# Performance work log

Hardware: AMD Instinct MI355X
Metric: run time of the kernel (lower is better)

## Reference

```python
import jax, jax.numpy as jnp
import numpy as np
from jax import lax

BN_EPS = 1e-5


def ternary_quantize(x):
    # thresholds from global max/min, split range into thirds
    mx, mn = jnp.max(x), jnp.min(x)
    lo = mn + (mx - mn) / 3
    hi = mx - (mx - mn) / 3
    return jnp.where(x < lo, -1.0, jnp.where(x > hi, 1.0, 0.0)).astype(x.dtype)


def noised_tri_conv(x, w):
    # w: [O, I, 3, 3]; bias=False in BasicBlock
    tw = w - jnp.mean(w)
    tq = ternary_quantize(tw)
    out = lax.conv_general_dilated(
        x, tq, window_strides=(1, 1), padding=((1, 1), (1, 1)),
        dimension_numbers=('NCHW', 'OIHW', 'NCHW'))
    # noised_forward: per-pixel conv of a 1x1 patch with padding=1 ->
    # only the center tap of the 3x3 kernel contributes; generated noise
    # weights are unused in the original code (faithful reproduction);
    # result is detached in torch.
    center = tq[:, :, 1, 1]  # [O, I]
    extra = lax.stop_gradient(jnp.einsum('bchw,oc->bohw', x, center))
    return out + extra


def batch_norm_train(x, gamma, beta):
    mean = jnp.mean(x, axis=(0, 2, 3), keepdims=True)
    var = jnp.var(x, axis=(0, 2, 3), keepdims=True)  # biased, as torch BN
    xhat = (x - mean) * lax.rsqrt(var + BN_EPS)
    return xhat * gamma[None, :, None, None] + beta[None, :, None, None]


def setup_inputs() -> dict:
    key = jax.random.key(0)
    k = jax.random.split(key, 7)
    C = 256
    x = jax.random.normal(k[0], (16, C, 56, 56), dtype=jnp.float32)
    w1 = jax.random.normal(k[1], (C, C, 3, 3), dtype=jnp.float32) * 0.05
    w2 = jax.random.normal(k[2], (C, C, 3, 3), dtype=jnp.float32) * 0.05
    g1 = jax.random.uniform(k[3], (C,), dtype=jnp.float32, minval=0.5, maxval=1.5)
    b1 = jax.random.normal(k[4], (C,), dtype=jnp.float32) * 0.1
    g2 = jax.random.uniform(k[5], (C,), dtype=jnp.float32, minval=0.5, maxval=1.5)
    b2 = jax.random.normal(k[6], (C,), dtype=jnp.float32) * 0.1
    return {'x': x, 'w1': w1, 'w2': w2, 'g1': g1, 'b1': b1, 'g2': g2, 'b2': b2}


def reference(x, w1, w2, g1, b1, g2, b2):
    out1 = noised_tri_conv(x, w1)
    out1 = batch_norm_train(out1, g1, b1)
    out1 = jax.nn.relu(out1)
    out2 = noised_tri_conv(out1, w2)
    out2 = batch_norm_train(out2, g2, b2)
    return jax.nn.relu(out1 + out2)
```

## Files before the change

kernel.cpp:

```cpp
#include <hip/hip_runtime.h>

typedef __bf16 bf16;
typedef __bf16 bf16x8 __attribute__((ext_vector_type(8)));
typedef float f32x4 __attribute__((ext_vector_type(4)));

#define NIMG 16
#define CCH 256
#define HH 56
#define HP 58
#define NBLK (NIMG * 14)
#define NPART 896
#define NPOSV (NIMG * HH * HH)
#define WELEMS 589824

typedef const __attribute__((address_space(1))) void* gas1_t;
typedef __attribute__((address_space(3))) void* las3_t;

__device__ __forceinline__ void gload16(const void* g, void* l) {
  __builtin_amdgcn_global_load_lds((gas1_t)g, (las3_t)l, 16, 0, 0);
}


__global__ __launch_bounds__(256) void w_partial(const float* __restrict__ w1,
                                                 const float* __restrict__ w2,
                                                 double* __restrict__ psum,
                                                 float* __restrict__ pmn,
                                                 float* __restrict__ pmx) {
  int b = blockIdx.x;
  int lb = b & 127;
  const float* w = (b >> 7) ? w2 : w1;
  int t = threadIdx.x;
  double s = 0.0;
  float mn = 3.4028235e38f, mx = -3.4028235e38f;
  for (int i = lb * 4608 + t; i < (lb + 1) * 4608; i += 256) {
    float v = w[i];
    s += (double)v;
    mn = fminf(mn, v);
    mx = fmaxf(mx, v);
  }
  __shared__ double sd[256];
  __shared__ float smn[256], smx[256];
  sd[t] = s; smn[t] = mn; smx[t] = mx;
  __syncthreads();
  for (int st = 128; st > 0; st >>= 1) {
    if (t < st) {
      sd[t] += sd[t + st];
      smn[t] = fminf(smn[t], smn[t + st]);
      smx[t] = fmaxf(smx[t], smx[t + st]);
    }
    __syncthreads();
  }
  if (t == 0) { psum[b] = sd[0]; pmn[b] = smn[0]; pmx[b] = smx[0]; }
}

__global__ void w_finalize(const double* __restrict__ psum,
                           const float* __restrict__ pmn,
                           const float* __restrict__ pmx,
                           float* __restrict__ wq) {
  int t = threadIdx.x;
  if (t < 2) {
    double s = 0.0;
    float mn = 3.4028235e38f, mx = -3.4028235e38f;
    for (int b = t * 128; b < (t + 1) * 128; b++) {
      s += psum[b];
      mn = fminf(mn, pmn[b]);
      mx = fmaxf(mx, pmx[b]);
    }
    float mean = (float)(s / (double)WELEMS);
    float tmn = mn - mean, tmx = mx - mean;
    float d = (tmx - tmn) / 3.0f;
    wq[t * 4 + 0] = mean;
    wq[t * 4 + 1] = tmn + d;
    wq[t * 4 + 2] = tmx - d;
  }
}

__global__ __launch_bounds__(256) void w_quant(const float* __restrict__ w1,
                                               const float* __restrict__ w2,
                                               const float* __restrict__ wq,
                                               bf16* __restrict__ btf1,
                                               bf16* __restrict__ btf2) {
  int bid = blockIdx.x;
  int widx = bid / 2304;
  const float* w = widx ? w2 : w1;
  bf16* bt = widx ? btf2 : btf1;
  float mean = wq[widx * 4], lo = wq[widx * 4 + 1], hi = wq[widx * 4 + 2];
  int e = (bid % 2304) * 256 + threadIdx.x;
  int ki = e & 7;
  int l = (e >> 3) & 63;
  int frag = e >> 9;
  int ob = frag & 15;
  int rest = frag >> 4;
  int kk = rest & 1;
  int scc = rest >> 1;
  int cc = scc & 3;
  int s = scc >> 2;
  int o = ob * 16 + (l & 15);
  int c = cc * 64 + kk * 32 + (l >> 4) * 8 + ki;
  float tv = w[(size_t)o * 2304 + c * 9 + s] - mean;
  float q = tv < lo ? -1.f : (tv > hi ? 1.f : 0.f);
  if (s == 4) q *= 2.f;
  bt[e] = (bf16)q;
}

__global__ __launch_bounds__(256) void pad_convert(const float* __restrict__ x,
                                                   bf16* __restrict__ xpad) {
  int bid = blockIdx.x;
  int hp = bid % HP;
  int n = bid / HP;
  int t = threadIdx.x;
  bf16* orow = xpad + (size_t)(n * HP + hp) * HP * CCH;
  bf16x8 z;
#pragma unroll
  for (int q = 0; q < 8; ++q) z[q] = (bf16)0.f;
  if (hp == 0 || hp == HP - 1) {
    for (int j = t; j < HP * 32; j += 256)
      *(bf16x8*)(orow + (size_t)(j >> 5) * CCH + (j & 31) * 8) = z;
    return;
  }
  __shared__ float tile[CCH * 57];
  const float* xb = x + (size_t)n * CCH * (HH * HH) + (size_t)(hp - 1) * HH;
  for (int j = t; j < CCH * 14; j += 256) {
    int c = j / 14, wq = j % 14;
    float4 v = *(const float4*)(xb + (size_t)c * (HH * HH) + wq * 4);
    float* tp = &tile[c * 57 + wq * 4];
    tp[0] = v.x; tp[1] = v.y; tp[2] = v.z; tp[3] = v.w;
  }
  __syncthreads();
  const int cg = t & 31;
  for (int j = t; j < HP * 32; j += 256) {
    int wp = j >> 5;
    bf16x8 ov = z;
    if (wp >= 1 && wp <= HH) {
#pragma unroll
      for (int q = 0; q < 8; ++q) ov[q] = (bf16)tile[(cg * 8 + q) * 57 + (wp - 1)];
    }
    *(bf16x8*)(orow + (size_t)wp * CCH + cg * 8) = ov;
  }
}

template <int MODE>
__global__ __launch_bounds__(512, 2) void conv_gemm(const bf16* __restrict__ xpad,
                                                    const bf16* __restrict__ btf,
                                                    float* __restrict__ part,
                                                    const bf16* __restrict__ v1pad,
                                                    const float* __restrict__ bnp,
                                                    float* __restrict__ outf,
                                                    bf16* __restrict__ outb) {
  __shared__ __align__(16) char smem[116736];
  const int t = threadIdx.x;
  const int lane = t & 63, wv = t >> 6;
  const int wm = wv >> 2, wn = wv & 3;
  const int g = lane >> 4, li = lane & 15;
  const int rawbid = blockIdx.x;
  const int bid = (rawbid & 7) * (NBLK / 8) + (rawbid >> 3);
  const int n = bid / 14, h0 = (bid % 14) * 4;

  f32x4 acc[8][4];
#pragma unroll
  for (int i = 0; i < 8; i++)
#pragma unroll
    for (int j = 0; j < 4; j++) acc[i][j] = f32x4{0.f, 0.f, 0.f, 0.f};

  auto stageA = [&](int cc, int b) {
#pragma unroll
    for (int i = 0; i < 6; ++i) {
      int idx = wv + i * 8;
      int rr = idx >> 3, po = idx & 7;
      int pp = po * 8 + (lane >> 3);
      int gs = (lane & 7) ^ (lane >> 3);
      const bf16* src = xpad + ((size_t)(n * HP + h0 + rr) * HP + pp) * CCH + cc * 64 + gs * 8;
      gload16(src, smem + b * 49152 + rr * 8192 + po * 1024 + lane * 16);
    }
  };

  auto loadB = [&](bf16x8 (&dst)[4], int s, int cc, int kk) {
#pragma unroll
    for (int f = 0; f < 4; ++f) {
      size_t fragidx = (size_t)(((s * 4 + cc) * 2 + kk) * 16 + wn * 4 + f);
      dst[f] = *(const bf16x8*)(btf + fragidx * 512 + lane * 8);
    }
  };

  auto compute_half = [&](const char* Ab, int half, int dh, int dw, int kk,
                          const bf16x8 (&bx)[4]) {
    bf16x8 a[4];
    int rr = 2 * wm + half + dh;
#pragma unroll
    for (int pc = 0; pc < 4; ++pc) {
      int p = pc * 16 + li + dw;
      int sl = (kk * 4 + g) ^ (p & 7);
      a[pc] = *(const bf16x8*)(Ab + rr * 8192 + p * 128 + sl * 16);
    }
#pragma unroll
    for (int pc = 0; pc < 4; ++pc)
#pragma unroll
      for (int fn = 0; fn < 4; ++fn)
        acc[half * 4 + pc][fn] =
          __builtin_amdgcn_mfma_f32_16x16x32_bf16(a[pc], bx[fn], acc[half * 4 + pc][fn], 0, 0, 0);
  };

  stageA(0, 0);
  bf16x8 bS[2][4];
  bf16x8 bB[4];
  loadB(bS[0], 0, 0, 0);
  __syncthreads();

#pragma unroll
  for (int cc = 0; cc < 4; ++cc) {
    const char* Ab = smem + (cc & 1) * 49152;
    if (cc < 3) stageA(cc + 1, (cc + 1) & 1);
#pragma unroll
    for (int s = 0; s < 9; ++s) {
      const int dh = s / 3, dw = s % 3;
      const int cur = (cc * 9 + s) & 1, nxt = cur ^ 1;
      if (s < 8) loadB(bS[nxt], s + 1, cc, 0);
      else if (cc < 3) loadB(bS[nxt], 0, cc + 1, 0);
      loadB(bB, s, cc, 1);
      __builtin_amdgcn_sched_barrier(0);
      __builtin_amdgcn_s_setprio(1);
      compute_half(Ab, 0, dh, dw, 0, bS[cur]);
      compute_half(Ab, 1, dh, dw, 0, bS[cur]);
      compute_half(Ab, 0, dh, dw, 1, bB);
      compute_half(Ab, 1, dh, dw, 1, bB);
      __builtin_amdgcn_s_setprio(0);
    }
    __syncthreads();
  }

  if (MODE == 1 || MODE == 3) {
    float so[2][4] = {{0.f,0.f,0.f,0.f},{0.f,0.f,0.f,0.f}};
    float qo[2][4] = {{0.f,0.f,0.f,0.f},{0.f,0.f,0.f,0.f}};
#pragma unroll
    for (int fm = 0; fm < 8; ++fm) {
      const int rl = fm >> 2, pc = fm & 3;
      const size_t rowoff = (size_t)(n * HH + h0 + 2 * wm + rl) * HH * CCH;
#pragma unroll
      for (int r = 0; r < 4; ++r) {
        int w = pc * 16 + g * 4 + r;
        if (w < HH) {
#pragma unroll
          for (int fn = 0; fn < 4; ++fn) {
            float v = acc[fm][fn][r];
            so[rl][fn] += v;
            qo[rl][fn] += v * v;
            if (MODE == 3) outb[rowoff + (size_t)w * CCH + wn * 64 + fn * 16 + li] = (bf16)v;
          }
        }
      }
    }
#pragma unroll
    for (int rl = 0; rl < 2; ++rl)
#pragma unroll
      for (int fn = 0; fn < 4; ++fn) {
        so[rl][fn] += __shfl_xor(so[rl][fn], 16);
        so[rl][fn] += __shfl_xor(so[rl][fn], 32);
        qo[rl][fn] += __shfl_xor(qo[rl][fn], 16);
        qo[rl][fn] += __shfl_xor(qo[rl][fn], 32);
      }
    if (g == 0) {
#pragma unroll
      for (int rl = 0; rl < 2; ++rl)
#pragma unroll
        for (int fn = 0; fn < 4; ++fn) {
          int o = wn * 64 + fn * 16 + lane;
          size_t prow = (size_t)(bid * 4 + 2 * wm + rl);
          part[(prow * CCH + o) * 2 + 0] = so[rl][fn];
          part[(prow * CCH + o) * 2 + 1] = qo[rl][fn];
        }
    }
  } else {
    float sc[4], bi[4];
#pragma unroll
    for (int fn = 0; fn < 4; ++fn) {
      int o = wn * 64 + fn * 16 + li;
      sc[fn] = bnp[o * 2];
      bi[fn] = bnp[o * 2 + 1];
    }
    float* fsm = (float*)smem;
    const int TS = 3648;
    for (int rl = 0; rl < 2; ++rl) {
      __syncthreads();
      const int row = h0 + 2 * wm + rl;
#pragma unroll
      for (int pc = 0; pc < 4; ++pc) {
        const int fm = rl * 4 + pc;
#pragma unroll
        for (int r = 0; r < 4; ++r) {
          int w = pc * 16 + g * 4 + r;
          if (w < HH) {
#pragma unroll
            for (int fn = 0; fn < 4; ++fn) {
              int o_loc = fn * 16 + li;
              fsm[wv * TS + w * 65 + o_loc] = acc[fm][fn][r] * sc[fn] + bi[fn];
            }
          }
        }
      }
      const bf16* v1row = v1pad + ((size_t)(n * HP + row + 1) * HP + 1) * CCH + wn * 64;
      for (int i = lane; i < HH * 8; i += 64) {
        int w = i >> 3, og = i & 7;
        bf16x8 v1v = *(const bf16x8*)(v1row + (size_t)w * CCH + og * 8);
        float* tp = &fsm[wv * TS + w * 65 + og * 8];
#pragma unroll
        for (int q = 0; q < 8; ++q) {
          float v = tp[q] + (float)v1v[q];
          tp[q] = v > 0.f ? v : 0.f;
        }
      }
      __syncthreads();
#pragma unroll
      for (int tl = 0; tl < 8; ++tl) {
        int wmt = tl >> 2, wnt = tl & 3;
        int orow = h0 + 2 * wmt + rl;
        for (int j = t; j < 4096; j += 512) {
          int oo = j >> 6, w = j & 63;
          if (w < HH)
            outf[(((size_t)n * CCH + wnt * 64 + oo) * HH + orow) * HH + w] = fsm[tl * TS + w * 65 + oo];
        }
      }
    }
  }
}

__global__ __launch_bounds__(256) void fuse2(const bf16* __restrict__ raw,
                                             const bf16* __restrict__ v1pad,
                                             const float* __restrict__ bnp,
                                             float* __restrict__ out) {
  __shared__ float tile[CCH * 57];
  int bid = blockIdx.x;
  int n = bid / HH, h = bid % HH;
  int t = threadIdx.x;
  const bf16* rrow = raw + (size_t)(n * HH + h) * HH * CCH;
  const bf16* vrow = v1pad + ((size_t)(n * HP + h + 1) * HP + 1) * CCH;
  const int cg = t & 31;
  float sc[8], bi[8];
#pragma unroll
  for (int q = 0; q < 8; ++q) {
    sc[q] = bnp[(cg * 8 + q) * 2];
    bi[q] = bnp[(cg * 8 + q) * 2 + 1];
  }
  for (int j = t; j < HH * 32; j += 256) {
    int w = j >> 5;
    bf16x8 r8 = *(const bf16x8*)(rrow + (size_t)w * CCH + cg * 8);
    bf16x8 v8 = *(const bf16x8*)(vrow + (size_t)w * CCH + cg * 8);
#pragma unroll
    for (int q = 0; q < 8; ++q) {
      float v = (float)r8[q] * sc[q] + bi[q] + (float)v8[q];
      tile[(cg * 8 + q) * 57 + w] = v > 0.f ? v : 0.f;
    }
  }
  __syncthreads();
  float* ob = out + (size_t)n * CCH * (HH * HH) + (size_t)h * HH;
  for (int j = t; j < CCH * 14; j += 256) {
    int c = j / 14, wq = j % 14;
    const float* tp = &tile[c * 57 + wq * 4];
    float4 v = {tp[0], tp[1], tp[2], tp[3]};
    *(float4*)(ob + (size_t)c * (HH * HH) + wq * 4) = v;
  }
}

__global__ __launch_bounds__(256) void bn_reduce1(const float* __restrict__ part,
                                                  float* __restrict__ part2) {
  int t = threadIdx.x, b = blockIdx.x;
  float s = 0.f, q = 0.f;
  for (int r = b * 28; r < (b + 1) * 28; r++) {
    s += part[((size_t)r * CCH + t) * 2 + 0];
    q += part[((size_t)r * CCH + t) * 2 + 1];
  }
  part2[((size_t)b * CCH + t) * 2 + 0] = s;
  part2[((size_t)b * CCH + t) * 2 + 1] = q;
}

__global__ __launch_bounds__(256) void bn_reduce2(const float* __restrict__ part2,
                                                  const float* __restrict__ gamma,
                                                  const float* __restrict__ beta,
                                                  float* __restrict__ params) {
  int t = threadIdx.x;
  float s = 0.f, q = 0.f;
  for (int b = 0; b < 32; b++) {
    s += part2[((size_t)b * CCH + t) * 2 + 0];
    q += part2[((size_t)b * CCH + t) * 2 + 1];
  }
  const float inv = 1.f / (float)NPOSV;
  float mean = s * inv;
  float var = q * inv - mean * mean;
  float sc = gamma[t] / sqrtf(var + 1e-5f);
  params[t * 2 + 0] = sc;
  params[t * 2 + 1] = beta[t] - mean * sc;
}

__global__ __launch_bounds__(256) void bn_apply_b(const bf16* __restrict__ rawb,
                                                  const float* __restrict__ params,
                                                  bf16* __restrict__ xpad) {
  int bid = blockIdx.x;
  int hp = bid % HP;
  int n = bid / HP;
  int t = threadIdx.x;
  bf16* orow = xpad + (size_t)(n * HP + hp) * HP * CCH;
  bf16x8 z;
#pragma unroll
  for (int q = 0; q < 8; ++q) z[q] = (bf16)0.f;
  if (hp == 0 || hp == HP - 1) {
    for (int j = t; j < HP * 32; j += 256)
      *(bf16x8*)(orow + (size_t)(j >> 5) * CCH + (j & 31) * 8) = z;
    return;
  }
  const int cg = t & 31, ws8 = t >> 5;
  float sc[8], bi[8];
#pragma unroll
  for (int q = 0; q < 8; ++q) {
    sc[q] = params[(cg * 8 + q) * 2];
    bi[q] = params[(cg * 8 + q) * 2 + 1];
  }
  const bf16* rrow = rawb + (size_t)(n * HH + (hp - 1)) * HH * CCH;
  for (int wp = ws8; wp < HP; wp += 8) {
    bf16x8 ov = z;
    if (wp >= 1 && wp <= HH) {
      bf16x8 r8 = *(const bf16x8*)(rrow + (size_t)(wp - 1) * CCH + cg * 8);
#pragma unroll
      for (int q = 0; q < 8; ++q) {
        float v = (float)r8[q] * sc[q] + bi[q];
        ov[q] = (bf16)(v > 0.f ? v : 0.f);
      }
    }
    *(bf16x8*)(orow + (size_t)wp * CCH + cg * 8) = ov;
  }
}


extern "C" void kernel_launch(void* const* d_in, const int* in_sizes, int n_in,
                              void* d_out, int out_size, void* d_ws, size_t ws_size,
                              hipStream_t stream) {
  const float* x  = (const float*)d_in[0];
  const float* w1 = (const float*)d_in[1];
  const float* w2 = (const float*)d_in[2];
  const float* g1 = (const float*)d_in[3];
  const float* b1 = (const float*)d_in[4];
  const float* g2 = (const float*)d_in[5];
  const float* b2 = (const float*)d_in[6];
  float* out = (float*)d_out;
  char* ws = (char*)d_ws;

  constexpr size_t O_BT1  = 0;
  constexpr size_t O_BT2  = O_BT1 + 1179648;
  constexpr size_t O_XPAD = O_BT2 + 1179648;
  constexpr size_t O_PART = O_XPAD + (size_t)NIMG * HP * HP * CCH * 2 + 65536;
  constexpr size_t O_PSUM = O_PART + (size_t)NPART * CCH * 2 * 4;
  constexpr size_t O_PMN  = O_PSUM + 2048;
  constexpr size_t O_PMX  = O_PMN + 1024;
  constexpr size_t O_WQ   = O_PMX + 1024;
  constexpr size_t O_BNP1 = O_WQ + 256;
  constexpr size_t O_BNP2 = O_BNP1 + 2048;
  constexpr size_t O_PART2 = O_BNP2 + 2048;
  constexpr size_t O_OUT2RAW = O_PART2 + 65536;
  constexpr size_t NEED_BIG = O_OUT2RAW + (size_t)NPOSV * CCH * 2 + 65536;

  bf16* bt1 = (bf16*)(ws + O_BT1);
  bf16* bt2 = (bf16*)(ws + O_BT2);
  bf16* xpad = (bf16*)(ws + O_XPAD);
  bf16* out1pad = (bf16*)(ws + O_XPAD);
  float* part = (float*)(ws + O_PART);
  double* psum = (double*)(ws + O_PSUM);
  float* pmn = (float*)(ws + O_PMN);
  float* pmx = (float*)(ws + O_PMX);
  float* wq = (float*)(ws + O_WQ);
  float* bnp1 = (float*)(ws + O_BNP1);
  float* bnp2 = (float*)(ws + O_BNP2);
  float* part2 = (float*)(ws + O_PART2);
  bf16* out2raw = (bf16*)(ws + O_OUT2RAW);
  bf16* out1rawb = (bf16*)d_out;

  w_partial<<<256, 256, 0, stream>>>(w1, w2, psum, pmn, pmx);
  w_finalize<<<1, 64, 0, stream>>>(psum, pmn, pmx, wq);
  w_quant<<<4608, 256, 0, stream>>>(w1, w2, wq, bt1, bt2);
  pad_convert<<<NIMG * HP, 256, 0, stream>>>(x, xpad);
  conv_gemm<3><<<NBLK, 512, 0, stream>>>(xpad, bt1, part, nullptr, nullptr, nullptr, out1rawb);
  bn_reduce1<<<32, 256, 0, stream>>>(part, part2);
  bn_reduce2<<<1, 256, 0, stream>>>(part2, g1, b1, bnp1);
  bn_apply_b<<<NIMG * HP, 256, 0, stream>>>(out1rawb, bnp1, out1pad);
  if (ws_size >= NEED_BIG) {
    conv_gemm<3><<<NBLK, 512, 0, stream>>>(out1pad, bt2, part, nullptr, nullptr, nullptr, out2raw);
    bn_reduce1<<<32, 256, 0, stream>>>(part, part2);
    bn_reduce2<<<1, 256, 0, stream>>>(part2, g2, b2, bnp2);
    fuse2<<<NIMG * HH, 256, 0, stream>>>(out2raw, out1pad, bnp2, out);
  } else {
    conv_gemm<1><<<NBLK, 512, 0, stream>>>(out1pad, bt2, part, nullptr, nullptr, nullptr, nullptr);
    bn_reduce1<<<32, 256, 0, stream>>>(part, part2);
    bn_reduce2<<<1, 256, 0, stream>>>(part2, g2, b2, bnp2);
    conv_gemm<2><<<NBLK, 512, 0, stream>>>(out1pad, bt2, nullptr, out1pad, bnp2, out, nullptr);
  }
}
```

Measured before the change: 192.0 us.

## Fuse BN statistics and apply into conv kernel via grid-wide spin barrier

Each conv kernel now keeps its accumulators in registers. After computing the tile, all blocks sync on a global atomic counter, the first 32 blocks reduce the partial BN sums, and a second counter barrier follows. Every block then derives the BN scale and bias itself and writes the normalized, ReLU'd result directly: padded bf16 in place for conv1, and the fp32 output with the residual for conv2. This drops the raw bf16 intermediate writes and reads, the separate reduce, apply and fuse kernels, and the conv recompute fallback path. It relies on all 224 blocks being co-resident, otherwise the spin barriers deadlock, and it adds spin-wait latency.

```diff
diff --git a/kernel.cpp b/kernel.cpp
--- a/kernel.cpp
+++ b/kernel.cpp
@@ -12,6 +12,7 @@
 #define NPART 896
 #define NPOSV (NIMG * HH * HH)
 #define WELEMS 589824
+#define NRED 32
 
 typedef const __attribute__((address_space(1))) void* gas1_t;
 typedef __attribute__((address_space(3))) void* las3_t;
@@ -19,6 +20,8 @@
 __device__ __forceinline__ void gload16(const void* g, void* l) {
   __builtin_amdgcn_global_load_lds((gas1_t)g, (las3_t)l, 16, 0, 0);
 }
+
+__global__ void zero_cnt(unsigned* c) { c[threadIdx.x] = 0u; }
 
 
 __global__ __launch_bounds__(256) void w_partial(const float* __restrict__ w1,
@@ -140,13 +143,17 @@
 }
 
 template <int MODE>
-__global__ __launch_bounds__(512, 2) void conv_gemm(const bf16* __restrict__ xpad,
+__global__ __launch_bounds__(512, 2) void conv_coop(const bf16* __restrict__ xpad,
                                                     const bf16* __restrict__ btf,
                                                     float* __restrict__ part,
+                                                    float* __restrict__ part2,
+                                                    const float* __restrict__ gamma,
+                                                    const float* __restrict__ beta,
                                                     const bf16* __restrict__ v1pad,
-                                                    const float* __restrict__ bnp,
+                                                    bf16* __restrict__ outb,
                                                     float* __restrict__ outf,
-                                                    bf16* __restrict__ outb) {
+                                                    unsigned* __restrict__ cnt_a,
+                                                    unsigned* __restrict__ cnt_b) {
   __shared__ __align__(16) char smem[116736];
   const int t = threadIdx.x;
   const int lane = t & 63, wv = t >> 6;
@@ -228,13 +235,12 @@
     __syncthreads();
   }
 
-  if (MODE == 1 || MODE == 3) {
+  {
     float so[2][4] = {{0.f,0.f,0.f,0.f},{0.f,0.f,0.f,0.f}};
     float qo[2][4] = {{0.f,0.f,0.f,0.f},{0.f,0.f,0.f,0.f}};
 #pragma unroll
     for (int fm = 0; fm < 8; ++fm) {
       const int rl = fm >> 2, pc = fm & 3;
-      const size_t rowoff = (size_t)(n * HH + h0 + 2 * wm + rl) * HH * CCH;
 #pragma unroll
       for (int r = 0; r < 4; ++r) {
         int w = pc * 16 + g * 4 + r;
@@ -244,7 +250,6 @@
             float v = acc[fm][fn][r];
             so[rl][fn] += v;
             qo[rl][fn] += v * v;
-            if (MODE == 3) outb[rowoff + (size_t)w * CCH + wn * 64 + fn * 16 + li] = (bf16)v;
           }
         }
       }
@@ -269,14 +274,77 @@
           part[(prow * CCH + o) * 2 + 1] = qo[rl][fn];
         }
     }
+  }
+
+  __syncthreads();
+  if (t == 0) {
+    __threadfence();
+    atomicAdd(cnt_a, 1u);
+  }
+  if (rawbid < NRED) {
+    if (t == 0) {
+      while (atomicAdd(cnt_a, 0u) < (unsigned)NBLK) __builtin_amdgcn_s_sleep(2);
+      __threadfence();
+    }
+    __syncthreads();
+    if (t < 256) {
+      float s = 0.f, q = 0.f;
+      for (int r = rawbid * 28; r < (rawbid + 1) * 28; r++) {
+        s += part[((size_t)r * CCH + t) * 2 + 0];
+        q += part[((size_t)r * CCH + t) * 2 + 1];
+      }
+      part2[((size_t)rawbid * CCH + t) * 2 + 0] = s;
+      part2[((size_t)rawbid * CCH + t) * 2 + 1] = q;
+    }
+    __syncthreads();
+    if (t == 0) {
+      __threadfence();
+      atomicAdd(cnt_b, 1u);
+    }
+  }
+  if (t == 0) {
+    while (atomicAdd(cnt_b, 0u) < (unsigned)NRED) __builtin_amdgcn_s_sleep(2);
+    __threadfence();
+  }
+  __syncthreads();
+
+  float sc[4], bi[4];
+  const float inv = 1.f / (float)NPOSV;
+#pragma unroll
+  for (int fn = 0; fn < 4; ++fn) {
+    int o = wn * 64 + fn * 16 + li;
+    float s = 0.f, q = 0.f;
+    for (int b = 0; b < NRED; ++b) {
+      s += part2[((size_t)b * CCH + o) * 2 + 0];
+      q += part2[((size_t)b * CCH + o) * 2 + 1];
+    }
+    float mean = s * inv;
+    float var = q * inv - mean * mean;
+    float scale = gamma[o] / sqrtf(var + 1e-5f);
+    sc[fn] = scale;
+    bi[fn] = beta[o] - mean * scale;
+  }
+
+  if (MODE == 1) {
+#pragma unroll
+    for (int fm = 0; fm < 8; ++fm) {
+      const int rl = fm >> 2, pc = fm & 3;
+      const int h = h0 + 2 * wm + rl;
+      bf16* obase = outb + ((size_t)(n * HP + h + 1) * HP + 1) * CCH;
+#pragma unroll
+      for (int r = 0; r < 4; ++r) {
+        int w = pc * 16 + g * 4 + r;
+        if (w < HH) {
+#pragma unroll
+          for (int fn = 0; fn < 4; ++fn) {
+            float v = acc[fm][fn][r] * sc[fn] + bi[fn];
+            v = v > 0.f ? v : 0.f;
+            obase[(size_t)w * CCH + wn * 64 + fn * 16 + li] = (bf16)v;
+          }
+        }
+      }
+    }
   } else {
-    float sc[4], bi[4];
-#pragma unroll
-    for (int fn = 0; fn < 4; ++fn) {
-      int o = wn * 64 + fn * 16 + li;
-      sc[fn] = bnp[o * 2];
-      bi[fn] = bnp[o * 2 + 1];
-    }
     float* fsm = (float*)smem;
     const int TS = 3648;
     for (int rl = 0; rl < 2; ++rl) {
@@ -320,111 +388,6 @@
         }
       }
     }
-  }
-}
-
-__global__ __launch_bounds__(256) void fuse2(const bf16* __restrict__ raw,
-                                             const bf16* __restrict__ v1pad,
-                                             const float* __restrict__ bnp,
-                                             float* __restrict__ out) {
-  __shared__ float tile[CCH * 57];
-  int bid = blockIdx.x;
-  int n = bid / HH, h = bid % HH;
-  int t = threadIdx.x;
-  const bf16* rrow = raw + (size_t)(n * HH + h) * HH * CCH;
-  const bf16* vrow = v1pad + ((size_t)(n * HP + h + 1) * HP + 1) * CCH;
-  const int cg = t & 31;
-  float sc[8], bi[8];
-#pragma unroll
-  for (int q = 0; q < 8; ++q) {
-    sc[q] = bnp[(cg * 8 + q) * 2];
-    bi[q] = bnp[(cg * 8 + q) * 2 + 1];
-  }
-  for (int j = t; j < HH * 32; j += 256) {
-    int w = j >> 5;
-    bf16x8 r8 = *(const bf16x8*)(rrow + (size_t)w * CCH + cg * 8);
-    bf16x8 v8 = *(const bf16x8*)(vrow + (size_t)w * CCH + cg * 8);
-#pragma unroll
-    for (int q = 0; q < 8; ++q) {
-      float v = (float)r8[q] * sc[q] + bi[q] + (float)v8[q];
-      tile[(cg * 8 + q) * 57 + w] = v > 0.f ? v : 0.f;
-    }
-  }
-  __syncthreads();
-  float* ob = out + (size_t)n * CCH * (HH * HH) + (size_t)h * HH;
-  for (int j = t; j < CCH * 14; j += 256) {
-    int c = j / 14, wq = j % 14;
-    const float* tp = &tile[c * 57 + wq * 4];
-    float4 v = {tp[0], tp[1], tp[2], tp[3]};
-    *(float4*)(ob + (size_t)c * (HH * HH) + wq * 4) = v;
-  }
-}
-
-__global__ __launch_bounds__(256) void bn_reduce1(const float* __restrict__ part,
-                                                  float* __restrict__ part2) {
-  int t = threadIdx.x, b = blockIdx.x;
-  float s = 0.f, q = 0.f;
-  for (int r = b * 28; r < (b + 1) * 28; r++) {
-    s += part[((size_t)r * CCH + t) * 2 + 0];
-    q += part[((size_t)r * CCH + t) * 2 + 1];
-  }
-  part2[((size_t)b * CCH + t) * 2 + 0] = s;
-  part2[((size_t)b * CCH + t) * 2 + 1] = q;
-}
-
-__global__ __launch_bounds__(256) void bn_reduce2(const float* __restrict__ part2,
-                                                  const float* __restrict__ gamma,
-                                                  const float* __restrict__ beta,
-                                                  float* __restrict__ params) {
-  int t = threadIdx.x;
-  float s = 0.f, q = 0.f;
-  for (int b = 0; b < 32; b++) {
-    s += part2[((size_t)b * CCH + t) * 2 + 0];
-    q += part2[((size_t)b * CCH + t) * 2 + 1];
-  }
-  const float inv = 1.f / (float)NPOSV;
-  float mean = s * inv;
-  float var = q * inv - mean * mean;
-  float sc = gamma[t] / sqrtf(var + 1e-5f);
-  params[t * 2 + 0] = sc;
-  params[t * 2 + 1] = beta[t] - mean * sc;
-}
-
-__global__ __launch_bounds__(256) void bn_apply_b(const bf16* __restrict__ rawb,
-                                                  const float* __restrict__ params,
-                                                  bf16* __restrict__ xpad) {
-  int bid = blockIdx.x;
-  int hp = bid % HP;
-  int n = bid / HP;
-  int t = threadIdx.x;
-  bf16* orow = xpad + (size_t)(n * HP + hp) * HP * CCH;
-  bf16x8 z;
-#pragma unroll
-  for (int q = 0; q < 8; ++q) z[q] = (bf16)0.f;
-  if (hp == 0 || hp == HP - 1) {
-    for (int j = t; j < HP * 32; j += 256)
-      *(bf16x8*)(orow + (size_t)(j >> 5) * CCH + (j & 31) * 8) = z;
-    return;
-  }
-  const int cg = t & 31, ws8 = t >> 5;
-  float sc[8], bi[8];
-#pragma unroll
-  for (int q = 0; q < 8; ++q) {
-    sc[q] = params[(cg * 8 + q) * 2];
-    bi[q] = params[(cg * 8 + q) * 2 + 1];
-  }
-  const bf16* rrow = rawb + (size_t)(n * HH + (hp - 1)) * HH * CCH;
-  for (int wp = ws8; wp < HP; wp += 8) {
-    bf16x8 ov = z;
-    if (wp >= 1 && wp <= HH) {
-      bf16x8 r8 = *(const bf16x8*)(rrow + (size_t)(wp - 1) * CCH + cg * 8);
-#pragma unroll
-      for (int q = 0; q < 8; ++q) {
-        float v = (float)r8[q] * sc[q] + bi[q];
-        ov[q] = (bf16)(v > 0.f ? v : 0.f);
-      }
-    }
-    *(bf16x8*)(orow + (size_t)wp * CCH + cg * 8) = ov;
   }
 }
 
@@ -450,44 +413,27 @@
   constexpr size_t O_PMN  = O_PSUM + 2048;
   constexpr size_t O_PMX  = O_PMN + 1024;
   constexpr size_t O_WQ   = O_PMX + 1024;
-  constexpr size_t O_BNP1 = O_WQ + 256;
-  constexpr size_t O_BNP2 = O_BNP1 + 2048;
-  constexpr size_t O_PART2 = O_BNP2 + 2048;
-  constexpr size_t O_OUT2RAW = O_PART2 + 65536;
-  constexpr size_t NEED_BIG = O_OUT2RAW + (size_t)NPOSV * CCH * 2 + 65536;
+  constexpr size_t O_PART2 = O_WQ + 256;
+  constexpr size_t O_CNT  = O_PART2 + 65536;
 
   bf16* bt1 = (bf16*)(ws + O_BT1);
   bf16* bt2 = (bf16*)(ws + O_BT2);
   bf16* xpad = (bf16*)(ws + O_XPAD);
-  bf16* out1pad = (bf16*)(ws + O_XPAD);
   float* part = (float*)(ws + O_PART);
   double* psum = (double*)(ws + O_PSUM);
   float* pmn = (float*)(ws + O_PMN);
   float* pmx = (float*)(ws + O_PMX);
   float* wq = (float*)(ws + O_WQ);
-  float* bnp1 = (float*)(ws + O_BNP1);
-  float* bnp2 = (float*)(ws + O_BNP2);
   float* part2 = (float*)(ws + O_PART2);
-  bf16* out2raw = (bf16*)(ws + O_OUT2RAW);
-  bf16* out1rawb = (bf16*)d_out;
-
+  unsigned* cnt = (unsigned*)(ws + O_CNT);
+
+  zero_cnt<<<1, 4, 0, stream>>>(cnt);
   w_partial<<<256, 256, 0, stream>>>(w1, w2, psum, pmn, pmx);
   w_finalize<<<1, 64, 0, stream>>>(psum, pmn, pmx, wq);
   w_quant<<<4608, 256, 0, stream>>>(w1, w2, wq, bt1, bt2);
   pad_convert<<<NIMG * HP, 256, 0, stream>>>(x, xpad);
-  conv_gemm<3><<<NBLK, 512, 0, stream>>>(xpad, bt1, part, nullptr, nullptr, nullptr, out1rawb);
-  bn_reduce1<<<32, 256, 0, stream>>>(part, part2);
-  bn_reduce2<<<1, 256, 0, stream>>>(part2, g1, b1, bnp1);
-  bn_apply_b<<<NIMG * HP, 256, 0, stream>>>(out1rawb, bnp1, out1pad);
-  if (ws_size >= NEED_BIG) {
-    conv_gemm<3><<<NBLK, 512, 0, stream>>>(out1pad, bt2, part, nullptr, nullptr, nullptr, out2raw);
-    bn_reduce1<<<32, 256, 0, stream>>>(part, part2);
-    bn_reduce2<<<1, 256, 0, stream>>>(part2, g2, b2, bnp2);
-    fuse2<<<NIMG * HH, 256, 0, stream>>>(out2raw, out1pad, bnp2, out);
-  } else {
-    conv_gemm<1><<<NBLK, 512, 0, stream>>>(out1pad, bt2, part, nullptr, nullptr, nullptr, nullptr);
-    bn_reduce1<<<32, 256, 0, stream>>>(part, part2);
-    bn_reduce2<<<1, 256, 0, stream>>>(part2, g2, b2, bnp2);
-    conv_gemm<2><<<NBLK, 512, 0, stream>>>(out1pad, bt2, nullptr, out1pad, bnp2, out, nullptr);
-  }
-}
+  conv_coop<1><<<NBLK, 512, 0, stream>>>(xpad, bt1, part, part2, g1, b1,
+                                         nullptr, xpad, nullptr, cnt + 0, cnt + 1);
+  conv_coop<2><<<NBLK, 512, 0, stream>>>(xpad, bt2, part, part2, g2, b2,
+                                         xpad, nullptr, out, cnt + 2, cnt + 3);
+}
```

Result: slower. 241.0 us (+25.5%).

## Use 4-wave conv blocks with 128-wide per-wave output tiles, drop fallback path

Applied to the files above, without the earlier changes.

Changes the conv GEMM from 8 waves of 512 threads to 4 waves of 256 threads. Each wave now computes a 128-row by 128-column tile (8x8 MFMA fragments) instead of 128x64, so A fragments from LDS and B fragments are reused across twice as many MFMAs. The cost is 256 accumulator floats per lane plus larger B register buffers, with one block per CU and fewer waves to hide latency. The workspace-size fallback path and the MODE template are removed, so the large-workspace path always runs.

```diff
diff --git a/kernel.cpp b/kernel.cpp
--- a/kernel.cpp
+++ b/kernel.cpp
@@ -139,33 +139,29 @@
   }
 }
 
-template <int MODE>
-__global__ __launch_bounds__(512, 2) void conv_gemm(const bf16* __restrict__ xpad,
+__global__ __launch_bounds__(256, 1) void conv_gemm(const bf16* __restrict__ xpad,
                                                     const bf16* __restrict__ btf,
                                                     float* __restrict__ part,
-                                                    const bf16* __restrict__ v1pad,
-                                                    const float* __restrict__ bnp,
-                                                    float* __restrict__ outf,
                                                     bf16* __restrict__ outb) {
-  __shared__ __align__(16) char smem[116736];
+  __shared__ __align__(16) char smem[98304];
   const int t = threadIdx.x;
   const int lane = t & 63, wv = t >> 6;
-  const int wm = wv >> 2, wn = wv & 3;
+  const int wm = wv >> 1, wn = wv & 1;
   const int g = lane >> 4, li = lane & 15;
   const int rawbid = blockIdx.x;
   const int bid = (rawbid & 7) * (NBLK / 8) + (rawbid >> 3);
   const int n = bid / 14, h0 = (bid % 14) * 4;
 
-  f32x4 acc[8][4];
+  f32x4 acc[8][8];
 #pragma unroll
   for (int i = 0; i < 8; i++)
 #pragma unroll
-    for (int j = 0; j < 4; j++) acc[i][j] = f32x4{0.f, 0.f, 0.f, 0.f};
+    for (int j = 0; j < 8; j++) acc[i][j] = f32x4{0.f, 0.f, 0.f, 0.f};
 
   auto stageA = [&](int cc, int b) {
 #pragma unroll
-    for (int i = 0; i < 6; ++i) {
-      int idx = wv + i * 8;
+    for (int i = 0; i < 12; ++i) {
+      int idx = wv + i * 4;
       int rr = idx >> 3, po = idx & 7;
       int pp = po * 8 + (lane >> 3);
       int gs = (lane & 7) ^ (lane >> 3);
@@ -174,35 +170,34 @@
     }
   };
 
-  auto loadB = [&](bf16x8 (&dst)[4], int s, int cc, int kk) {
-#pragma unroll
-    for (int f = 0; f < 4; ++f) {
-      size_t fragidx = (size_t)(((s * 4 + cc) * 2 + kk) * 16 + wn * 4 + f);
+  auto loadB = [&](bf16x8 (&dst)[8], int s, int cc, int kk) {
+#pragma unroll
+    for (int f = 0; f < 8; ++f) {
+      size_t fragidx = (size_t)(((s * 4 + cc) * 2 + kk) * 16 + wn * 8 + f);
       dst[f] = *(const bf16x8*)(btf + fragidx * 512 + lane * 8);
     }
   };
 
-  auto compute_half = [&](const char* Ab, int half, int dh, int dw, int kk,
-                          const bf16x8 (&bx)[4]) {
-    bf16x8 a[4];
-    int rr = 2 * wm + half + dh;
-#pragma unroll
-    for (int pc = 0; pc < 4; ++pc) {
-      int p = pc * 16 + li + dw;
+  auto compute_kk = [&](const char* Ab, int dh, int dw, int kk, const bf16x8 (&bx)[8]) {
+    bf16x8 a[8];
+#pragma unroll
+    for (int pc = 0; pc < 8; ++pc) {
+      int rr = 2 * wm + (pc >> 2) + dh;
+      int p = (pc & 3) * 16 + li + dw;
       int sl = (kk * 4 + g) ^ (p & 7);
       a[pc] = *(const bf16x8*)(Ab + rr * 8192 + p * 128 + sl * 16);
     }
 #pragma unroll
-    for (int pc = 0; pc < 4; ++pc)
-#pragma unroll
-      for (int fn = 0; fn < 4; ++fn)
-        acc[half * 4 + pc][fn] =
-          __builtin_amdgcn_mfma_f32_16x16x32_bf16(a[pc], bx[fn], acc[half * 4 + pc][fn], 0, 0, 0);
+    for (int pc = 0; pc < 8; ++pc)
+#pragma unroll
+      for (int fn = 0; fn < 8; ++fn)
+        acc[pc][fn] =
+          __builtin_amdgcn_mfma_f32_16x16x32_bf16(a[pc], bx[fn], acc[pc][fn], 0, 0, 0);
   };
 
   stageA(0, 0);
-  bf16x8 bS[2][4];
-  bf16x8 bB[4];
+  bf16x8 bS[2][8];
+  bf16x8 bB[8];
   loadB(bS[0], 0, 0, 0);
   __syncthreads();
 
@@ -219,107 +214,55 @@
       loadB(bB, s, cc, 1);
       __builtin_amdgcn_sched_barrier(0);
       __builtin_amdgcn_s_setprio(1);
-      compute_half(Ab, 0, dh, dw, 0, bS[cur]);
-      compute_half(Ab, 1, dh, dw, 0, bS[cur]);
-      compute_half(Ab, 0, dh, dw, 1, bB);
-      compute_half(Ab, 1, dh, dw, 1, bB);
+      compute_kk(Ab, dh, dw, 0, bS[cur]);
+      compute_kk(Ab, dh, dw, 1, bB);
       __builtin_amdgcn_s_setprio(0);
     }
     __syncthreads();
   }
 
-  if (MODE == 1 || MODE == 3) {
-    float so[2][4] = {{0.f,0.f,0.f,0.f},{0.f,0.f,0.f,0.f}};
-    float qo[2][4] = {{0.f,0.f,0.f,0.f},{0.f,0.f,0.f,0.f}};
-#pragma unroll
-    for (int fm = 0; fm < 8; ++fm) {
-      const int rl = fm >> 2, pc = fm & 3;
-      const size_t rowoff = (size_t)(n * HH + h0 + 2 * wm + rl) * HH * CCH;
-#pragma unroll
-      for (int r = 0; r < 4; ++r) {
-        int w = pc * 16 + g * 4 + r;
-        if (w < HH) {
-#pragma unroll
-          for (int fn = 0; fn < 4; ++fn) {
-            float v = acc[fm][fn][r];
-            so[rl][fn] += v;
-            qo[rl][fn] += v * v;
-            if (MODE == 3) outb[rowoff + (size_t)w * CCH + wn * 64 + fn * 16 + li] = (bf16)v;
-          }
+  float so[2][8], qo[2][8];
+#pragma unroll
+  for (int rl = 0; rl < 2; ++rl)
+#pragma unroll
+    for (int fn = 0; fn < 8; ++fn) { so[rl][fn] = 0.f; qo[rl][fn] = 0.f; }
+#pragma unroll
+  for (int pc = 0; pc < 8; ++pc) {
+    const int rl = pc >> 2, pq = pc & 3;
+    const size_t rowoff = (size_t)(n * HH + h0 + 2 * wm + rl) * HH * CCH;
+#pragma unroll
+    for (int r = 0; r < 4; ++r) {
+      int w = pq * 16 + g * 4 + r;
+      if (w < HH) {
+#pragma unroll
+        for (int fn = 0; fn < 8; ++fn) {
+          float v = acc[pc][fn][r];
+          so[rl][fn] += v;
+          qo[rl][fn] += v * v;
+          outb[rowoff + (size_t)w * CCH + wn * 128 + fn * 16 + li] = (bf16)v;
         }
       }
     }
+  }
+#pragma unroll
+  for (int rl = 0; rl < 2; ++rl)
+#pragma unroll
+    for (int fn = 0; fn < 8; ++fn) {
+      so[rl][fn] += __shfl_xor(so[rl][fn], 16);
+      so[rl][fn] += __shfl_xor(so[rl][fn], 32);
+      qo[rl][fn] += __shfl_xor(qo[rl][fn], 16);
+      qo[rl][fn] += __shfl_xor(qo[rl][fn], 32);
+    }
+  if (g == 0) {
 #pragma unroll
     for (int rl = 0; rl < 2; ++rl)
 #pragma unroll
-      for (int fn = 0; fn < 4; ++fn) {
-        so[rl][fn] += __shfl_xor(so[rl][fn], 16);
-        so[rl][fn] += __shfl_xor(so[rl][fn], 32);
-        qo[rl][fn] += __shfl_xor(qo[rl][fn], 16);
-        qo[rl][fn] += __shfl_xor(qo[rl][fn], 32);
+      for (int fn = 0; fn < 8; ++fn) {
+        int o = wn * 128 + fn * 16 + lane;
+        size_t prow = (size_t)(bid * 4 + 2 * wm + rl);
+        part[(prow * CCH + o) * 2 + 0] = so[rl][fn];
+        part[(prow * CCH + o) * 2 + 1] = qo[rl][fn];
       }
-    if (g == 0) {
-#pragma unroll
-      for (int rl = 0; rl < 2; ++rl)
-#pragma unroll
-        for (int fn = 0; fn < 4; ++fn) {
-          int o = wn * 64 + fn * 16 + lane;
-          size_t prow = (size_t)(bid * 4 + 2 * wm + rl);
-          part[(prow * CCH + o) * 2 + 0] = so[rl][fn];
-          part[(prow * CCH + o) * 2 + 1] = qo[rl][fn];
-        }
-    }
-  } else {
-    float sc[4], bi[4];
-#pragma unroll
-    for (int fn = 0; fn < 4; ++fn) {
-      int o = wn * 64 + fn * 16 + li;
-      sc[fn] = bnp[o * 2];
-      bi[fn] = bnp[o * 2 + 1];
-    }
-    float* fsm = (float*)smem;
-    const int TS = 3648;
-    for (int rl = 0; rl < 2; ++rl) {
-      __syncthreads();
-      const int row = h0 + 2 * wm + rl;
-#pragma unroll
-      for (int pc = 0; pc < 4; ++pc) {
-        const int fm = rl * 4 + pc;
-#pragma unroll
-        for (int r = 0; r < 4; ++r) {
-          int w = pc * 16 + g * 4 + r;
-          if (w < HH) {
-#pragma unroll
-            for (int fn = 0; fn < 4; ++fn) {
-              int o_loc = fn * 16 + li;
-              fsm[wv * TS + w * 65 + o_loc] = acc[fm][fn][r] * sc[fn] + bi[fn];
-            }
-          }
-        }
-      }
-      const bf16* v1row = v1pad + ((size_t)(n * HP + row + 1) * HP + 1) * CCH + wn * 64;
-      for (int i = lane; i < HH * 8; i += 64) {
-        int w = i >> 3, og = i & 7;
-        bf16x8 v1v = *(const bf16x8*)(v1row + (size_t)w * CCH + og * 8);
-        float* tp = &fsm[wv * TS + w * 65 + og * 8];
-#pragma unroll
-        for (int q = 0; q < 8; ++q) {
-          float v = tp[q] + (float)v1v[q];
-          tp[q] = v > 0.f ? v : 0.f;
-        }
-      }
-      __syncthreads();
-#pragma unroll
-      for (int tl = 0; tl < 8; ++tl) {
-        int wmt = tl >> 2, wnt = tl & 3;
-        int orow = h0 + 2 * wmt + rl;
-        for (int j = t; j < 4096; j += 512) {
-          int oo = j >> 6, w = j & 63;
-          if (w < HH)
-            outf[(((size_t)n * CCH + wnt * 64 + oo) * HH + orow) * HH + w] = fsm[tl * TS + w * 65 + oo];
-        }
-      }
-    }
   }
 }
 
@@ -454,7 +397,6 @@
   constexpr size_t O_BNP2 = O_BNP1 + 2048;
   constexpr size_t O_PART2 = O_BNP2 + 2048;
   constexpr size_t O_OUT2RAW = O_PART2 + 65536;
-  constexpr size_t NEED_BIG = O_OUT2RAW + (size_t)NPOSV * CCH * 2 + 65536;
 
   bf16* bt1 = (bf16*)(ws + O_BT1);
   bf16* bt2 = (bf16*)(ws + O_BT2);
@@ -475,19 +417,12 @@
   w_finalize<<<1, 64, 0, stream>>>(psum, pmn, pmx, wq);
   w_quant<<<4608, 256, 0, stream>>>(w1, w2, wq, bt1, bt2);
   pad_convert<<<NIMG * HP, 256, 0, stream>>>(x, xpad);
-  conv_gemm<3><<<NBLK, 512, 0, stream>>>(xpad, bt1, part, nullptr, nullptr, nullptr, out1rawb);
+  conv_gemm<<<NBLK, 256, 0, stream>>>(xpad, bt1, part, out1rawb);
   bn_reduce1<<<32, 256, 0, stream>>>(part, part2);
   bn_reduce2<<<1, 256, 0, stream>>>(part2, g1, b1, bnp1);
   bn_apply_b<<<NIMG * HP, 256, 0, stream>>>(out1rawb, bnp1, out1pad);
-  if (ws_size >= NEED_BIG) {
-    conv_gemm<3><<<NBLK, 512, 0, stream>>>(out1pad, bt2, part, nullptr, nullptr, nullptr, out2raw);
-    bn_reduce1<<<32, 256, 0, stream>>>(part, part2);
-    bn_reduce2<<<1, 256, 0, stream>>>(part2, g2, b2, bnp2);
-    fuse2<<<NIMG * HH, 256, 0, stream>>>(out2raw, out1pad, bnp2, out);
-  } else {
-    conv_gemm<1><<<NBLK, 512, 0, stream>>>(out1pad, bt2, part, nullptr, nullptr, nullptr, nullptr);
-    bn_reduce1<<<32, 256, 0, stream>>>(part, part2);
-    bn_reduce2<<<1, 256, 0, stream>>>(part2, g2, b2, bnp2);
-    conv_gemm<2><<<NBLK, 512, 0, stream>>>(out1pad, bt2, nullptr, out1pad, bnp2, out, nullptr);
-  }
-}
+  conv_gemm<<<NBLK, 256, 0, stream>>>(out1pad, bt2, part, out2raw);
+  bn_reduce1<<<32, 256, 0, stream>>>(part, part2);
+  bn_reduce2<<<1, 256, 0, stream>>>(part2, g2, b2, bnp2);
+  fuse2<<<NIMG * HH, 256, 0, stream>>>(out2raw, out1pad, bnp2, out);
+}
```

Measured after the change: 219.7 us. 14.5% more time.
